# Performance work log

Measured on AMD Instinct MI355X. Metric: run time of the kernel, lower is better.

## Reference

```python
import jax, jax.numpy as jnp
import numpy as np
from jax import lax

N = 65536          # particles per arm
T_MAX = 10.0       # span of stripping times (natural units, GM=a=1)
GM = 1.0           # Hernquist mass parameter
A_SCALE = 1.0      # Hernquist scale radius


def setup_inputs() -> dict:
    key = jax.random.key(0)
    k1, k2, k3, k4, k5 = jax.random.split(key, 5)
    # sorted stripping times in [0, T_MAX)
    ts = jnp.sort(jax.random.uniform(k1, (N,), dtype=jnp.float32) * T_MAX)
    # lead/trail initial phase-space points: q ~ 1.5*N(0,1) kpc-ish, p ~ 0.3*N(0,1)
    q_l = 1.5 * jax.random.normal(k2, (N, 3), dtype=jnp.float32)
    p_l = 0.3 * jax.random.normal(k3, (N, 3), dtype=jnp.float32)
    q_t = 1.5 * jax.random.normal(k4, (N, 3), dtype=jnp.float32)
    p_t = 0.3 * jax.random.normal(k5, (N, 3), dtype=jnp.float32)
    return {
        "ts": ts,
        "w0_lead": jnp.concatenate([q_l, p_l], axis=-1),
        "w0_trail": jnp.concatenate([q_t, p_t], axis=-1),
        "n_steps": 64,
    }


def _accel(q):
    # Hernquist acceleration: -GM * r_vec / (r * (r + a)^2); bounded as r -> 0.
    r = jnp.sqrt(jnp.sum(q * q, axis=-1, keepdims=True))
    return -GM * q / (r * (r + A_SCALE) ** 2 + 1e-12)


def _integrate_batch(w0, dt, n_steps):
    # w0: [N,6], dt: [N]  -- every lane takes n_steps (max-steps semantics of
    # the vmapped adaptive solver), leapfrog kick-drift-kick.
    q, p = w0[:, :3], w0[:, 3:]
    dt_ = dt[:, None]

    def step(carry, _):
        q, p = carry
        p_half = p + 0.5 * dt_ * _accel(q)
        q_new = q + dt_ * p_half
        p_new = p_half + 0.5 * dt_ * _accel(q_new)
        return (q_new, p_new), None

    (qf, pf), _ = lax.scan(step, (q, p), None, length=n_steps)
    return jnp.concatenate([qf, pf], axis=-1)  # [N,6]


def reference(ts, w0_lead, w0_trail, n_steps):
    # per-particle integration window [ts[i], t_f], t_f = ts[-1] + 0.001
    t_f = ts[-1] + jnp.asarray(0.001, ts.dtype)
    dt = (t_f - ts) / n_steps  # [N]
    w_lead = _integrate_batch(w0_lead, dt, n_steps)    # [N,6]
    w_trail = _integrate_batch(w0_trail, dt, n_steps)  # [N,6]
    # interleave_concat(trail, lead, axis=0): trail[0], lead[0], trail[1], ...
    w = jnp.stack([w_trail, w_lead], axis=1).reshape(2 * w_lead.shape[0], 6)
    return w
```

## Files before the change

### kernel.cpp

```cpp
#include <hip/hip_runtime.h>
#include <hip/hip_bf16.h>


#define N_PART 65536

__device__ __forceinline__ void accel(float qx, float qy, float qz,
                                      float& ax, float& ay, float& az) {
    float r2 = qx * qx + qy * qy + qz * qz;
    float r  = sqrtf(r2);
    float rp = r + 1.0f;
    float denom = r * rp * rp + 1e-12f;
    float inv = -1.0f / denom;
    ax = qx * inv;
    ay = qy * inv;
    az = qz * inv;
}

__global__ void __launch_bounds__(256)
leapfrog_kernel(const float* __restrict__ ts,
                const float* __restrict__ w0_lead,
                const float* __restrict__ w0_trail,
                const int* __restrict__ n_steps_p,
                float* __restrict__ out) {
    const int tid = blockIdx.x * blockDim.x + threadIdx.x;
    if (tid >= 2 * N_PART) return;

    const int i       = tid >> 1;
    const int is_lead = tid & 1;

    const float* __restrict__ src = is_lead ? w0_lead : w0_trail;

    const float t_f = ts[N_PART - 1] + 0.001f;
    const int n_steps = *n_steps_p;
    const float dt  = (t_f - ts[i]) / (float)n_steps;
    const float hdt = 0.5f * dt;

    const long base = (long)i * 6;
    float qx = src[base + 0];
    float qy = src[base + 1];
    float qz = src[base + 2];
    float px = src[base + 3];
    float py = src[base + 4];
    float pz = src[base + 5];

    float ax, ay, az;
    accel(qx, qy, qz, ax, ay, az);

    for (int s = 0; s < n_steps; ++s) {
        const float phx = px + hdt * ax;
        const float phy = py + hdt * ay;
        const float phz = pz + hdt * az;
        qx += dt * phx;
        qy += dt * phy;
        qz += dt * phz;
        accel(qx, qy, qz, ax, ay, az);
        px = phx + hdt * ax;
        py = phy + hdt * ay;
        pz = phz + hdt * az;
    }

    const long obase = (long)tid * 6;
    out[obase + 0] = qx;
    out[obase + 1] = qy;
    out[obase + 2] = qz;
    out[obase + 3] = px;
    out[obase + 4] = py;
    out[obase + 5] = pz;
}

extern "C" void kernel_launch(void* const* d_in, const int* in_sizes, int n_in,
                              void* d_out, int out_size, void* d_ws, size_t ws_size,
                              hipStream_t stream) {
    const float* ts       = (const float*)d_in[0];
    const float* w0_lead  = (const float*)d_in[1];
    const float* w0_trail = (const float*)d_in[2];
    const int*   n_steps  = (const int*)d_in[3];
    float* out = (float*)d_out;

    const int total = 2 * N_PART;
    const int block = 256;
    const int grid  = (total + block - 1) / block;

    leapfrog_kernel<<<grid, block, 0, stream>>>(ts, w0_lead, w0_trail, n_steps, out);
}
```

Baseline: 71.39 us.

## Merge leapfrog half-kicks into full kicks and use fast sqrt/rcp intrinsics

Rewrites the kick-drift-kick loop so consecutive half-kicks merge into one full kick, with a half-kick peeled at the start and end. This drops one set of velocity updates per step. The acceleration now uses hardware sqrt and reciprocal builtins and FMAs instead of an IEEE divide, and the loop is unrolled by 4. The cost is small numerical differences from the approximate reciprocal and from the reordered arithmetic.

```diff
diff --git a/kernel.cpp b/kernel.cpp
--- a/kernel.cpp
+++ b/kernel.cpp
@@ -4,16 +4,12 @@
 
 #define N_PART 65536
 
-__device__ __forceinline__ void accel(float qx, float qy, float qz,
-                                      float& ax, float& ay, float& az) {
-    float r2 = qx * qx + qy * qy + qz * qz;
-    float r  = sqrtf(r2);
+__device__ __forceinline__ float neg_inv_denom(float qx, float qy, float qz) {
+    float r2 = fmaf(qx, qx, fmaf(qy, qy, qz * qz));
+    float r  = __builtin_amdgcn_sqrtf(r2);
     float rp = r + 1.0f;
-    float denom = r * rp * rp + 1e-12f;
-    float inv = -1.0f / denom;
-    ax = qx * inv;
-    ay = qy * inv;
-    az = qz * inv;
+    float d  = fmaf(r * rp, rp, 1e-12f);
+    return -__builtin_amdgcn_rcpf(d);
 }
 
 __global__ void __launch_bounds__(256)
@@ -30,10 +26,10 @@
 
     const float* __restrict__ src = is_lead ? w0_lead : w0_trail;
 
-    const float t_f = ts[N_PART - 1] + 0.001f;
-    const int n_steps = *n_steps_p;
-    const float dt  = (t_f - ts[i]) / (float)n_steps;
-    const float hdt = 0.5f * dt;
+    const float t_f     = ts[N_PART - 1] + 0.001f;
+    const int   n_steps = *n_steps_p;
+    const float dt      = (t_f - ts[i]) / (float)n_steps;
+    const float hdt     = 0.5f * dt;
 
     const long base = (long)i * 6;
     float qx = src[base + 0];
@@ -43,21 +39,29 @@
     float py = src[base + 4];
     float pz = src[base + 5];
 
-    float ax, ay, az;
-    accel(qx, qy, qz, ax, ay, az);
+    float c  = hdt * neg_inv_denom(qx, qy, qz);
+    float phx = fmaf(c, qx, px);
+    float phy = fmaf(c, qy, py);
+    float phz = fmaf(c, qz, pz);
 
-    for (int s = 0; s < n_steps; ++s) {
-        const float phx = px + hdt * ax;
-        const float phy = py + hdt * ay;
-        const float phz = pz + hdt * az;
-        qx += dt * phx;
-        qy += dt * phy;
-        qz += dt * phz;
-        accel(qx, qy, qz, ax, ay, az);
-        px = phx + hdt * ax;
-        py = phy + hdt * ay;
-        pz = phz + hdt * az;
+    #pragma unroll 4
+    for (int s = 0; s < n_steps - 1; ++s) {
+        qx = fmaf(dt, phx, qx);
+        qy = fmaf(dt, phy, qy);
+        qz = fmaf(dt, phz, qz);
+        c  = dt * neg_inv_denom(qx, qy, qz);
+        phx = fmaf(c, qx, phx);
+        phy = fmaf(c, qy, phy);
+        phz = fmaf(c, qz, phz);
     }
+
+    qx = fmaf(dt, phx, qx);
+    qy = fmaf(dt, phy, qy);
+    qz = fmaf(dt, phz, qz);
+    c  = hdt * neg_inv_denom(qx, qy, qz);
+    px = fmaf(c, qx, phx);
+    py = fmaf(c, qy, phy);
+    pz = fmaf(c, qz, phz);
 
     const long obase = (long)tid * 6;
     out[obase + 0] = qx;
```

Measured after the change: 63.87 us. 1.12x faster.
